# Optimization experiments

Measured on AMD Instinct MI355X. Metric: run time of the kernel, lower is better.

Reference implementation:

```python
import jax, jax.numpy as jnp
import numpy as np

D_MODEL = 1024
D_STATE = 16
D_CONV = 4
D_INNER = 2 * D_MODEL
DT_RANK = (D_MODEL + 15) // 16  # 64
BATCH = 4
SEQ = 1024
LN_EPS = 1e-5


def setup_inputs() -> dict:
    key = jax.random.key(0)
    ks = jax.random.split(key, 16)
    s = 0.02
    inp = {
        "query": jax.random.normal(ks[0], (BATCH, SEQ, D_MODEL), jnp.float32),
        "diff_ts": jax.random.normal(ks[1], (BATCH, D_MODEL), jnp.float32),
        # AdaLN modulation Linear (2*D, D) + bias (zero-init in source; random here to exercise math)
        "adaln_w": jax.random.normal(ks[2], (2 * D_MODEL, D_MODEL), jnp.float32) * s,
        "adaln_b": jax.random.normal(ks[3], (2 * D_MODEL,), jnp.float32) * s,
        # Mamba params
        "w_in": jax.random.normal(ks[4], (2 * D_INNER, D_MODEL), jnp.float32) * s,
        "conv_w": jax.random.normal(ks[5], (D_INNER, D_CONV), jnp.float32) * s,
        "conv_b": jax.random.normal(ks[6], (D_INNER,), jnp.float32) * s,
        "w_xproj": jax.random.normal(ks[7], (DT_RANK + 2 * D_STATE, D_INNER), jnp.float32) * s,
        "w_dt": jax.random.normal(ks[8], (D_INNER, DT_RANK), jnp.float32) * s,
        # dt bias such that softplus(b_dt) is small/positive (Mamba-style init)
        "b_dt": jnp.log(jnp.expm1(jax.random.uniform(ks[9], (D_INNER,), jnp.float32, 1e-3, 0.1))),
        # A_log = log(1..d_state) per channel (official Mamba S4D-real init)
        "a_log": jnp.log(jnp.tile(jnp.arange(1, D_STATE + 1, dtype=jnp.float32), (D_INNER, 1))),
        "d_skip": jnp.ones((D_INNER,), jnp.float32),
        "w_out": jax.random.normal(ks[10], (D_MODEL, D_INNER), jnp.float32) * s,
        "ln_g": jnp.ones((D_MODEL,), jnp.float32),
        "ln_b": jnp.zeros((D_MODEL,), jnp.float32),
    }
    return inp


def _mamba(x, w_in, conv_w, conv_b, w_xproj, w_dt, b_dt, a_log, d_skip, w_out):
    B, L, _ = x.shape
    xz = jnp.einsum("bld,ed->ble", x, w_in)          # (B, L, 2*d_inner)
    u, z = jnp.split(xz, 2, axis=-1)                   # each (B, L, d_inner)

    # causal depthwise conv1d over L (d_conv taps)
    up = jnp.pad(u, ((0, 0), (D_CONV - 1, 0), (0, 0)))
    uc = conv_b
    uc = sum(up[:, k:k + L, :] * conv_w[:, k] for k in range(D_CONV)) + conv_b
    u = jax.nn.silu(uc)                                # (B, L, d_inner)

    x_dbl = jnp.einsum("bld,ed->ble", u, w_xproj)      # (B, L, dt_rank + 2*d_state)
    dt = x_dbl[..., :DT_RANK]
    Bm = x_dbl[..., DT_RANK:DT_RANK + D_STATE]         # (B, L, d_state)
    Cm = x_dbl[..., DT_RANK + D_STATE:]                # (B, L, d_state)

    delta = jax.nn.softplus(jnp.einsum("blr,dr->bld", dt, w_dt) + b_dt)  # (B, L, d_inner)
    A = -jnp.exp(a_log)                                # (d_inner, d_state)

    def step(h, xs):
        d_t, B_t, C_t, u_t = xs                        # (B,d_inner),(B,ds),(B,ds),(B,d_inner)
        dA = jnp.exp(d_t[..., None] * A)               # (B, d_inner, d_state)
        h = dA * h + (d_t * u_t)[..., None] * B_t[:, None, :]
        y = jnp.einsum("bds,bs->bd", h, C_t)
        return h, y

    h0 = jnp.zeros((B, D_INNER, D_STATE), u.dtype)
    xs = (delta.transpose(1, 0, 2), Bm.transpose(1, 0, 2),
          Cm.transpose(1, 0, 2), u.transpose(1, 0, 2))
    _, ys = jax.lax.scan(step, h0, xs)                 # ys: (L, B, d_inner)
    y = ys.transpose(1, 0, 2) + u * d_skip
    y = y * jax.nn.silu(z)
    return jnp.einsum("bld,ed->ble", y, w_out)         # (B, L, d_model)


def reference(query, diff_ts, adaln_w, adaln_b, w_in, conv_w, conv_b,
              w_xproj, w_dt, b_dt, a_log, d_skip, w_out, ln_g, ln_b):
    # AdaLN: SiLU -> Linear -> chunk into scale/shift
    mod = jax.nn.silu(diff_ts) @ adaln_w.T + adaln_b   # (B, 2*D)
    scale, shift = jnp.split(mod, 2, axis=-1)
    aq = query * (1.0 + scale[:, None, :]) + shift[:, None, :]

    attn = _mamba(aq, w_in, conv_w, conv_b, w_xproj, w_dt, b_dt, a_log, d_skip, w_out)
    out = query + attn                                 # dropout p=0 (eval)

    mu = jnp.mean(out, axis=-1, keepdims=True)
    var = jnp.var(out, axis=-1, keepdims=True)
    return (out - mu) * jax.lax.rsqrt(var + LN_EPS) * ln_g + ln_b
```

## Files before the change

kernel.cpp:

```cpp
#include <hip/hip_runtime.h>
#include <hip/hip_bf16.h>

typedef __attribute__((ext_vector_type(8))) short short8;
typedef __attribute__((ext_vector_type(4))) float f32x4;

union B4 { __hip_bfloat16 h[4]; uint2 v; };
union B8 { __hip_bfloat16 h[8]; short8 s; };

__global__ void __launch_bounds__(256) k_adaln_mod(const float* __restrict__ dts,
                                                   const float* __restrict__ w,
                                                   const float* __restrict__ b,
                                                   float* __restrict__ mod) {
    __shared__ float sd[1024];
    int bb = blockIdx.x >> 3;
    int e  = ((blockIdx.x & 7) << 8) + threadIdx.x;
    for (int i = threadIdx.x; i < 1024; i += 256) {
        float x = dts[bb * 1024 + i];
        sd[i] = x / (1.f + __expf(-x));
    }
    __syncthreads();
    const float* wr = w + (size_t)e * 1024;
    float acc = 0.f;
    for (int k = 0; k < 1024; k += 4) {
        float4 wv = *(const float4*)(wr + k);
        acc += wv.x * sd[k] + wv.y * sd[k + 1] + wv.z * sd[k + 2] + wv.w * sd[k + 3];
    }
    mod[bb * 2048 + e] = acc + b[e];
}

__global__ void __launch_bounds__(256) k_modulate(const float* __restrict__ q,
                                                  const float* __restrict__ mod,
                                                  __hip_bfloat16* __restrict__ aq) {
    int idx = blockIdx.x * 256 + threadIdx.x;
    int m = idx >> 8, o = (idx & 255) << 2;
    int bb = m >> 10;
    float4 qv = *(const float4*)(q + (size_t)m * 1024 + o);
    float4 sc = *(const float4*)(mod + bb * 2048 + o);
    float4 sh = *(const float4*)(mod + bb * 2048 + 1024 + o);
    B4 t;
    t.h[0] = __float2bfloat16(qv.x * (1.f + sc.x) + sh.x);
    t.h[1] = __float2bfloat16(qv.y * (1.f + sc.y) + sh.y);
    t.h[2] = __float2bfloat16(qv.z * (1.f + sc.z) + sh.z);
    t.h[3] = __float2bfloat16(qv.w * (1.f + sc.w) + sh.w);
    *(uint2*)(aq + (size_t)m * 1024 + o) = t.v;
}

__global__ void __launch_bounds__(256) k_cast(const float* __restrict__ in,
                                              __hip_bfloat16* __restrict__ out, int n4) {
    int i = blockIdx.x * 256 + threadIdx.x;
    if (i >= n4) return;
    float4 v = ((const float4*)in)[i];
    B4 t;
    t.h[0] = __float2bfloat16(v.x); t.h[1] = __float2bfloat16(v.y);
    t.h[2] = __float2bfloat16(v.z); t.h[3] = __float2bfloat16(v.w);
    ((uint2*)out)[i] = t.v;
}

__global__ void __launch_bounds__(256) k_cast_pad_xproj(const float* __restrict__ in,
                                                        __hip_bfloat16* __restrict__ out) {
    int i = blockIdx.x * 256 + threadIdx.x;
    int e = i >> 9, o = (i & 511) << 2;
    float4 v = make_float4(0.f, 0.f, 0.f, 0.f);
    if (e < 96) v = *(const float4*)&in[e * 2048 + o];
    B4 t;
    t.h[0] = __float2bfloat16(v.x); t.h[1] = __float2bfloat16(v.y);
    t.h[2] = __float2bfloat16(v.z); t.h[3] = __float2bfloat16(v.w);
    *(uint2*)&out[e * 2048 + o] = t.v;
}

__global__ void __launch_bounds__(256) k_cast_dt(const float* __restrict__ x_dbl,
                                                 __hip_bfloat16* __restrict__ dt) {
    int i = blockIdx.x * 256 + threadIdx.x;
    int m = i >> 4, o = (i & 15) << 2;
    float4 v = *(const float4*)&x_dbl[m * 128 + o];
    B4 t;
    t.h[0] = __float2bfloat16(v.x); t.h[1] = __float2bfloat16(v.y);
    t.h[2] = __float2bfloat16(v.z); t.h[3] = __float2bfloat16(v.w);
    *(uint2*)&dt[m * 64 + o] = t.v;
}

template <int EPI>
__global__ void __launch_bounds__(256) k_gemm_nt(const __hip_bfloat16* __restrict__ A, int lda,
                                                 const __hip_bfloat16* __restrict__ B, int ldb,
                                                 float* __restrict__ Cf,
                                                 __hip_bfloat16* __restrict__ Cb, int ldc,
                                                 int K, const float* __restrict__ ep) {
    __shared__ short As[128 * 40];
    __shared__ short Bs[128 * 40];
    int tid = threadIdx.x;
    int lane = tid & 63, wid = tid >> 6;
    int row0 = blockIdx.y << 7, col0 = blockIdx.x << 7;
    int wm = (wid >> 1) << 6, wn = (wid & 1) << 6;
    int fr = lane & 15, ko = (lane >> 4) << 3;

    int ra0 = tid >> 2, oa = (tid & 3) << 3;
    int ra1 = ra0 + 64;

    const short* Ag = (const short*)A;
    const short* Bg = (const short*)B;

    f32x4 acc[4][4] = {};

    for (int k0 = 0; k0 < K; k0 += 32) {
        __syncthreads();
        *(short8*)&As[ra0 * 40 + oa] = *(const short8*)&Ag[(size_t)(row0 + ra0) * lda + k0 + oa];
        *(short8*)&As[ra1 * 40 + oa] = *(const short8*)&Ag[(size_t)(row0 + ra1) * lda + k0 + oa];
        *(short8*)&Bs[ra0 * 40 + oa] = *(const short8*)&Bg[(size_t)(col0 + ra0) * ldb + k0 + oa];
        *(short8*)&Bs[ra1 * 40 + oa] = *(const short8*)&Bg[(size_t)(col0 + ra1) * ldb + k0 + oa];
        __syncthreads();
        short8 a[4], b[4];
#pragma unroll
        for (int mi = 0; mi < 4; ++mi) a[mi] = *(const short8*)&As[(wm + mi * 16 + fr) * 40 + ko];
#pragma unroll
        for (int ni = 0; ni < 4; ++ni) b[ni] = *(const short8*)&Bs[(wn + ni * 16 + fr) * 40 + ko];
#pragma unroll
        for (int mi = 0; mi < 4; ++mi)
#pragma unroll
            for (int ni = 0; ni < 4; ++ni)
                acc[mi][ni] = __builtin_amdgcn_mfma_f32_16x16x32_bf16(a[mi], b[ni], acc[mi][ni], 0, 0, 0);
    }

    int er = (lane >> 4) << 2;
    int ec = lane & 15;
#pragma unroll
    for (int mi = 0; mi < 4; ++mi)
#pragma unroll
        for (int ni = 0; ni < 4; ++ni)
#pragma unroll
            for (int r = 0; r < 4; ++r) {
                int gr = row0 + wm + mi * 16 + er + r;
                int gc = col0 + wn + ni * 16 + ec;
                size_t off = (size_t)gr * ldc + gc;
                float v = acc[mi][ni][r];
                if (EPI == 0) {
                    Cb[off] = __float2bfloat16(v);
                } else if (EPI == 1) {
                    Cf[off] = v;
                } else if (EPI == 2) {
                    float x = v + ep[gc];
                    Cf[off] = (x > 20.f) ? x : log1pf(__expf(x));
                } else {
                    Cf[off] = v + ep[off];
                }
            }
}

__global__ void __launch_bounds__(256) k_conv(const __hip_bfloat16* __restrict__ xz,
                                              const float* __restrict__ cw,
                                              const float* __restrict__ cb,
                                              __hip_bfloat16* __restrict__ u_act) {
    int idx = blockIdx.x * 256 + threadIdx.x;
    int m = idx >> 8, d = (idx & 255) << 3;
    int l = m & 1023;
    float acc[8];
#pragma unroll
    for (int j = 0; j < 8; ++j) acc[j] = cb[d + j];
#pragma unroll
    for (int k = 0; k < 4; ++k) {
        int lt = l - 3 + k;
        if (lt < 0) continue;
        B8 v;
        v.s = *(const short8*)(xz + (size_t)(m - 3 + k) * 4096 + d);
#pragma unroll
        for (int j = 0; j < 8; ++j)
            acc[j] += __bfloat162float(v.h[j]) * cw[(d + j) * 4 + k];
    }
    B8 o;
#pragma unroll
    for (int j = 0; j < 8; ++j) {
        float x = acc[j];
        o.h[j] = __float2bfloat16(x / (1.f + __expf(-x)));
    }
    *(short8*)(u_act + (size_t)m * 2048 + d) = o.s;
}

__global__ void __launch_bounds__(256) k_scan_p1(const float* __restrict__ delta,
                                                 const __hip_bfloat16* __restrict__ u_act,
                                                 const float* __restrict__ x_dbl,
                                                 const float* __restrict__ a_log,
                                                 float* __restrict__ chP,
                                                 float* __restrict__ chS) {
    int tid = threadIdx.x;
    int bid = blockIdx.x;
    int bb = bid >> 7;
    int c  = (bid >> 3) & 15;
    int dg = bid & 7;
    int d  = (dg << 8) + tid;
    float A2[16], P[16], h[16];
#pragma unroll
    for (int s = 0; s < 16; ++s) {
        A2[s] = -__expf(a_log[d * 16 + s]) * 1.44269504f;
        P[s] = 1.f;
        h[s] = 0.f;
    }
    int m0 = (bb << 10) + (c << 6);
    for (int t = 0; t < 64; ++t) {
        int m = m0 + t;
        float dt = delta[(size_t)m * 2048 + d];
        float uv = __bfloat162float(u_act[(size_t)m * 2048 + d]);
        float x = dt * uv;
        const float* Brow = x_dbl + (size_t)m * 128 + 64;
#pragma unroll
        for (int s = 0; s < 16; ++s) {
            float dA = exp2f(dt * A2[s]);
            P[s] *= dA;
            h[s] = fmaf(dA, h[s], x * Brow[s]);
        }
    }
    size_t base = (size_t)((bb * 16 + c) * 16) * 2048 + d;
#pragma unroll
    for (int s = 0; s < 16; ++s) {
        chP[base + (size_t)s * 2048] = P[s];
        chS[base + (size_t)s * 2048] = h[s];
    }
}

__global__ void __launch_bounds__(256) k_scan_p2(const float* __restrict__ chP,
                                                 float* __restrict__ chS) {
    int idx = blockIdx.x * 256 + threadIdx.x;
    int bb = idx >> 15;
    int s  = (idx >> 11) & 15;
    int d  = idx & 2047;
    float h = 0.f;
    for (int c = 0; c < 16; ++c) {
        size_t off = (size_t)((bb * 16 + c) * 16 + s) * 2048 + d;
        float Pv = chP[off];
        float Sv = chS[off];
        chS[off] = h;
        h = fmaf(Pv, h, Sv);
    }
}

__global__ void __launch_bounds__(256) k_scan_p3(const float* __restrict__ delta,
                                                 const __hip_bfloat16* __restrict__ u_act,
                                                 const __hip_bfloat16* __restrict__ xz,
                                                 const float* __restrict__ x_dbl,
                                                 const float* __restrict__ a_log,
                                                 const float* __restrict__ d_skip,
                                                 const float* __restrict__ hinit,
                                                 __hip_bfloat16* __restrict__ y) {
    int tid = threadIdx.x;
    int bid = blockIdx.x;
    int bb = bid >> 7;
    int c  = (bid >> 3) & 15;
    int dg = bid & 7;
    int d  = (dg << 8) + tid;
    float A2[16], h[16];
    size_t base = (size_t)((bb * 16 + c) * 16) * 2048 + d;
#pragma unroll
    for (int s = 0; s < 16; ++s) {
        A2[s] = -__expf(a_log[d * 16 + s]) * 1.44269504f;
        h[s] = hinit[base + (size_t)s * 2048];
    }
    float dsk = d_skip[d];
    int m0 = (bb << 10) + (c << 6);
    for (int t = 0; t < 64; ++t) {
        int m = m0 + t;
        float dt = delta[(size_t)m * 2048 + d];
        float uv = __bfloat162float(u_act[(size_t)m * 2048 + d]);
        float x = dt * uv;
        const float* Brow = x_dbl + (size_t)m * 128 + 64;
        const float* Crow = Brow + 16;
        float yacc = 0.f;
#pragma unroll
        for (int s = 0; s < 16; ++s) {
            float dA = exp2f(dt * A2[s]);
            h[s] = fmaf(dA, h[s], x * Brow[s]);
            yacc = fmaf(h[s], Crow[s], yacc);
        }
        float zv = __bfloat162float(xz[(size_t)m * 4096 + 2048 + d]);
        float yv = (yacc + uv * dsk) * (zv / (1.f + __expf(-zv)));
        y[(size_t)m * 2048 + d] = __float2bfloat16(yv);
    }
}

__global__ void __launch_bounds__(256) k_ln(float* __restrict__ out,
                                            const float* __restrict__ g,
                                            const float* __restrict__ b) {
    int row = blockIdx.x;
    float* p = out + (size_t)row * 1024;
    int tid = threadIdx.x;
    float4 v = ((float4*)p)[tid];
    float s1 = v.x + v.y + v.z + v.w;
    float s2 = v.x * v.x + v.y * v.y + v.z * v.z + v.w * v.w;
    for (int off = 1; off < 64; off <<= 1) {
        s1 += __shfl_xor(s1, off, 64);
        s2 += __shfl_xor(s2, off, 64);
    }
    __shared__ float a1[4], a2[4];
    int wid = tid >> 6;
    if ((tid & 63) == 0) { a1[wid] = s1; a2[wid] = s2; }
    __syncthreads();
    s1 = a1[0] + a1[1] + a1[2] + a1[3];
    s2 = a2[0] + a2[1] + a2[2] + a2[3];
    float mean = s1 * (1.f / 1024.f);
    float var = s2 * (1.f / 1024.f) - mean * mean;
    float inv = rsqrtf(var + 1e-5f);
    float4 gv = ((const float4*)g)[tid];
    float4 bv = ((const float4*)b)[tid];
    v.x = (v.x - mean) * inv * gv.x + bv.x;
    v.y = (v.y - mean) * inv * gv.y + bv.y;
    v.z = (v.z - mean) * inv * gv.z + bv.z;
    v.w = (v.w - mean) * inv * gv.w + bv.w;
    ((float4*)p)[tid] = v;
}

extern "C" void kernel_launch(void* const* d_in, const int* in_sizes, int n_in,
                              void* d_out, int out_size, void* d_ws, size_t ws_size,
                              hipStream_t stream) {
    const float* query   = (const float*)d_in[0];
    const float* diff_ts = (const float*)d_in[1];
    const float* adaln_w = (const float*)d_in[2];
    const float* adaln_b = (const float*)d_in[3];
    const float* w_in    = (const float*)d_in[4];
    const float* conv_w  = (const float*)d_in[5];
    const float* conv_b  = (const float*)d_in[6];
    const float* w_xproj = (const float*)d_in[7];
    const float* w_dt    = (const float*)d_in[8];
    const float* b_dt    = (const float*)d_in[9];
    const float* a_log   = (const float*)d_in[10];
    const float* d_skip  = (const float*)d_in[11];
    const float* w_out   = (const float*)d_in[12];
    const float* ln_g    = (const float*)d_in[13];
    const float* ln_b    = (const float*)d_in[14];
    float* out = (float*)d_out;

    char* w = (char*)d_ws;
    auto alloc = [&](size_t bytes) -> char* {
        char* p = w;
        w += (bytes + 255) & ~(size_t)255;
        return p;
    };
    float*          mod     = (float*)         alloc((size_t)4 * 2048 * 4);
    __hip_bfloat16* aq      = (__hip_bfloat16*)alloc((size_t)4096 * 1024 * 2);
    __hip_bfloat16* w_in_b  = (__hip_bfloat16*)alloc((size_t)4096 * 1024 * 2);
    __hip_bfloat16* w_out_b = (__hip_bfloat16*)alloc((size_t)1024 * 2048 * 2);
    __hip_bfloat16* w_xp_b  = (__hip_bfloat16*)alloc((size_t)128 * 2048 * 2);
    __hip_bfloat16* w_dt_b  = (__hip_bfloat16*)alloc((size_t)2048 * 64 * 2);
    __hip_bfloat16* xz      = (__hip_bfloat16*)alloc((size_t)4096 * 4096 * 2);
    __hip_bfloat16* u_act   = (__hip_bfloat16*)alloc((size_t)4096 * 2048 * 2);
    float*          x_dbl   = (float*)         alloc((size_t)4096 * 128 * 4);
    __hip_bfloat16* dtb     = (__hip_bfloat16*)alloc((size_t)4096 * 64 * 2);
    float*          delta   = (float*)         alloc((size_t)4096 * 2048 * 4);
    __hip_bfloat16* yb      = (__hip_bfloat16*)alloc((size_t)4096 * 2048 * 2);
    float*          chP     = (float*)         alloc((size_t)4 * 16 * 16 * 2048 * 4);
    float*          chS     = (float*)         alloc((size_t)4 * 16 * 16 * 2048 * 4);

    k_adaln_mod<<<32, 256, 0, stream>>>(diff_ts, adaln_w, adaln_b, mod);
    k_modulate<<<4096, 256, 0, stream>>>(query, mod, aq);
    k_cast<<<4096, 256, 0, stream>>>(w_in, w_in_b, 4096 * 1024 / 4);
    k_cast<<<2048, 256, 0, stream>>>(w_out, w_out_b, 1024 * 2048 / 4);
    k_cast_pad_xproj<<<256, 256, 0, stream>>>(w_xproj, w_xp_b);
    k_cast<<<128, 256, 0, stream>>>(w_dt, w_dt_b, 2048 * 64 / 4);

    k_gemm_nt<0><<<dim3(32, 32), 256, 0, stream>>>(aq, 1024, w_in_b, 1024,
                                                   nullptr, xz, 4096, 1024, nullptr);
    k_conv<<<4096, 256, 0, stream>>>(xz, conv_w, conv_b, u_act);
    k_gemm_nt<1><<<dim3(1, 32), 256, 0, stream>>>(u_act, 2048, w_xp_b, 2048,
                                                  x_dbl, nullptr, 128, 2048, nullptr);
    k_cast_dt<<<256, 256, 0, stream>>>(x_dbl, dtb);
    k_gemm_nt<2><<<dim3(16, 32), 256, 0, stream>>>(dtb, 64, w_dt_b, 64,
                                                   delta, nullptr, 2048, 64, b_dt);
    k_scan_p1<<<512, 256, 0, stream>>>(delta, u_act, x_dbl, a_log, chP, chS);
    k_scan_p2<<<512, 256, 0, stream>>>(chP, chS);
    k_scan_p3<<<512, 256, 0, stream>>>(delta, u_act, xz, x_dbl, a_log, d_skip, chS, yb);
    k_gemm_nt<3><<<dim3(8, 32), 256, 0, stream>>>(yb, 2048, w_out_b, 2048,
                                                  out, nullptr, 1024, 2048, query);
    k_ln<<<4096, 256, 0, stream>>>(out, ln_g, ln_b);
}
```

Baseline: 532.7 us.

## Double scan chunk count and stage B/C rows in shared memory

Splits the chunked selective scan into 32 chunks of 32 steps instead of 16 chunks of 64, doubling the block count of the first and third scan passes to improve occupancy and parallelism on the GPU. Each block preloads its B and C rows from x_dbl into LDS and reads them as vector loads, replacing repeated scalar global loads. In exchange, the carry pass walks twice as many chunks and the chunk state buffers double in size.

```diff
diff --git a/kernel.cpp b/kernel.cpp
--- a/kernel.cpp
+++ b/kernel.cpp
@@ -180,12 +180,18 @@
                                                  const float* __restrict__ a_log,
                                                  float* __restrict__ chP,
                                                  float* __restrict__ chS) {
+    __shared__ __align__(16) float sBC[32][32];
     int tid = threadIdx.x;
     int bid = blockIdx.x;
-    int bb = bid >> 7;
-    int c  = (bid >> 3) & 15;
+    int bb = bid >> 8;
+    int c  = (bid >> 3) & 31;
     int dg = bid & 7;
     int d  = (dg << 8) + tid;
+    int m0 = (bb << 10) + (c << 5);
+    {
+        int r = tid >> 3, q = (tid & 7) << 2;
+        *(float4*)&sBC[r][q] = *(const float4*)&x_dbl[(size_t)(m0 + r) * 128 + 64 + q];
+    }
     float A2[16], P[16], h[16];
 #pragma unroll
     for (int s = 0; s < 16; ++s) {
@@ -193,21 +199,25 @@
         P[s] = 1.f;
         h[s] = 0.f;
     }
-    int m0 = (bb << 10) + (c << 6);
-    for (int t = 0; t < 64; ++t) {
+    __syncthreads();
+    for (int t = 0; t < 32; ++t) {
         int m = m0 + t;
         float dt = delta[(size_t)m * 2048 + d];
         float uv = __bfloat162float(u_act[(size_t)m * 2048 + d]);
         float x = dt * uv;
-        const float* Brow = x_dbl + (size_t)m * 128 + 64;
+        f32x4 Bv0 = *(const f32x4*)&sBC[t][0];
+        f32x4 Bv1 = *(const f32x4*)&sBC[t][4];
+        f32x4 Bv2 = *(const f32x4*)&sBC[t][8];
+        f32x4 Bv3 = *(const f32x4*)&sBC[t][12];
 #pragma unroll
         for (int s = 0; s < 16; ++s) {
+            float Bs_ = (s < 4) ? Bv0[s & 3] : (s < 8) ? Bv1[s & 3] : (s < 12) ? Bv2[s & 3] : Bv3[s & 3];
             float dA = exp2f(dt * A2[s]);
             P[s] *= dA;
-            h[s] = fmaf(dA, h[s], x * Brow[s]);
+            h[s] = fmaf(dA, h[s], x * Bs_);
         }
     }
-    size_t base = (size_t)((bb * 16 + c) * 16) * 2048 + d;
+    size_t base = (size_t)((bb * 32 + c) * 16) * 2048 + d;
 #pragma unroll
     for (int s = 0; s < 16; ++s) {
         chP[base + (size_t)s * 2048] = P[s];
@@ -222,8 +232,8 @@
     int s  = (idx >> 11) & 15;
     int d  = idx & 2047;
     float h = 0.f;
-    for (int c = 0; c < 16; ++c) {
-        size_t off = (size_t)((bb * 16 + c) * 16 + s) * 2048 + d;
+    for (int c = 0; c < 32; ++c) {
+        size_t off = (size_t)((bb * 32 + c) * 16 + s) * 2048 + d;
         float Pv = chP[off];
         float Sv = chS[off];
         chS[off] = h;
@@ -239,34 +249,48 @@
                                                  const float* __restrict__ d_skip,
                                                  const float* __restrict__ hinit,
                                                  __hip_bfloat16* __restrict__ y) {
+    __shared__ __align__(16) float sBC[32][32];
     int tid = threadIdx.x;
     int bid = blockIdx.x;
-    int bb = bid >> 7;
-    int c  = (bid >> 3) & 15;
+    int bb = bid >> 8;
+    int c  = (bid >> 3) & 31;
     int dg = bid & 7;
     int d  = (dg << 8) + tid;
+    int m0 = (bb << 10) + (c << 5);
+    {
+        int r = tid >> 3, q = (tid & 7) << 2;
+        *(float4*)&sBC[r][q] = *(const float4*)&x_dbl[(size_t)(m0 + r) * 128 + 64 + q];
+    }
     float A2[16], h[16];
-    size_t base = (size_t)((bb * 16 + c) * 16) * 2048 + d;
+    size_t base = (size_t)((bb * 32 + c) * 16) * 2048 + d;
 #pragma unroll
     for (int s = 0; s < 16; ++s) {
         A2[s] = -__expf(a_log[d * 16 + s]) * 1.44269504f;
         h[s] = hinit[base + (size_t)s * 2048];
     }
     float dsk = d_skip[d];
-    int m0 = (bb << 10) + (c << 6);
-    for (int t = 0; t < 64; ++t) {
+    __syncthreads();
+    for (int t = 0; t < 32; ++t) {
         int m = m0 + t;
         float dt = delta[(size_t)m * 2048 + d];
         float uv = __bfloat162float(u_act[(size_t)m * 2048 + d]);
         float x = dt * uv;
-        const float* Brow = x_dbl + (size_t)m * 128 + 64;
-        const float* Crow = Brow + 16;
+        f32x4 Bv0 = *(const f32x4*)&sBC[t][0];
+        f32x4 Bv1 = *(const f32x4*)&sBC[t][4];
+        f32x4 Bv2 = *(const f32x4*)&sBC[t][8];
+        f32x4 Bv3 = *(const f32x4*)&sBC[t][12];
+        f32x4 Cv0 = *(const f32x4*)&sBC[t][16];
+        f32x4 Cv1 = *(const f32x4*)&sBC[t][20];
+        f32x4 Cv2 = *(const f32x4*)&sBC[t][24];
+        f32x4 Cv3 = *(const f32x4*)&sBC[t][28];
         float yacc = 0.f;
 #pragma unroll
         for (int s = 0; s < 16; ++s) {
+            float Bs_ = (s < 4) ? Bv0[s & 3] : (s < 8) ? Bv1[s & 3] : (s < 12) ? Bv2[s & 3] : Bv3[s & 3];
+            float Cs_ = (s < 4) ? Cv0[s & 3] : (s < 8) ? Cv1[s & 3] : (s < 12) ? Cv2[s & 3] : Cv3[s & 3];
             float dA = exp2f(dt * A2[s]);
-            h[s] = fmaf(dA, h[s], x * Brow[s]);
-            yacc = fmaf(h[s], Crow[s], yacc);
+            h[s] = fmaf(dA, h[s], x * Bs_);
+            yacc = fmaf(h[s], Cs_, yacc);
         }
         float zv = __bfloat162float(xz[(size_t)m * 4096 + 2048 + d]);
         float yv = (yacc + uv * dsk) * (zv / (1.f + __expf(-zv)));
@@ -343,8 +367,8 @@
     __hip_bfloat16* dtb     = (__hip_bfloat16*)alloc((size_t)4096 * 64 * 2);
     float*          delta   = (float*)         alloc((size_t)4096 * 2048 * 4);
     __hip_bfloat16* yb      = (__hip_bfloat16*)alloc((size_t)4096 * 2048 * 2);
-    float*          chP     = (float*)         alloc((size_t)4 * 16 * 16 * 2048 * 4);
-    float*          chS     = (float*)         alloc((size_t)4 * 16 * 16 * 2048 * 4);
+    float*          chP     = (float*)         alloc((size_t)4 * 32 * 16 * 2048 * 4);
+    float*          chS     = (float*)         alloc((size_t)4 * 32 * 16 * 2048 * 4);
 
     k_adaln_mod<<<32, 256, 0, stream>>>(diff_ts, adaln_w, adaln_b, mod);
     k_modulate<<<4096, 256, 0, stream>>>(query, mod, aq);
@@ -361,9 +385,9 @@
     k_cast_dt<<<256, 256, 0, stream>>>(x_dbl, dtb);
     k_gemm_nt<2><<<dim3(16, 32), 256, 0, stream>>>(dtb, 64, w_dt_b, 64,
                                                    delta, nullptr, 2048, 64, b_dt);
-    k_scan_p1<<<512, 256, 0, stream>>>(delta, u_act, x_dbl, a_log, chP, chS);
+    k_scan_p1<<<1024, 256, 0, stream>>>(delta, u_act, x_dbl, a_log, chP, chS);
     k_scan_p2<<<512, 256, 0, stream>>>(chP, chS);
-    k_scan_p3<<<512, 256, 0, stream>>>(delta, u_act, xz, x_dbl, a_log, d_skip, chS, yb);
+    k_scan_p3<<<1024, 256, 0, stream>>>(delta, u_act, xz, x_dbl, a_log, d_skip, chS, yb);
     k_gemm_nt<3><<<dim3(8, 32), 256, 0, stream>>>(yb, 2048, w_out_b, 2048,
                                                   out, nullptr, 1024, 2048, query);
     k_ln<<<4096, 256, 0, stream>>>(out, ln_g, ln_b);
```

Result: faster. 513.7 us (-3.6%).
